# Performance work log

Hardware: AMD Instinct MI355X
Metric: run time of the kernel (lower is better)

The kernel has to match this reference:

```python
import jax, jax.numpy as jnp
import numpy as np

IMG = 640
STRIDES = (8, 16, 32)
A = 5            # anchors per level
NC = 80          # num classes
IOU_TH = 0.5
NEG_RATIO = 1.0


def make_priors():
    scales = [1.0, 1.5, 2.0, 2.5, 3.0]
    out = []
    for s in STRIDES:
        f = IMG // s
        ys, xs = np.meshgrid(np.arange(f), np.arange(f), indexing='ij')
        cx = ((xs + 0.5) / f).ravel()
        cy = ((ys + 0.5) / f).ravel()
        for sc in scales:  # anchor-major to match merge_features (A, h, w) order
            wh = min(sc * 4.0 * s / IMG, 1.0)
            out.append(np.stack([cx, cy, np.full_like(cx, wh), np.full_like(cx, wh)], 1))
    return np.concatenate(out, 0).astype(np.float32)  # [42000, 4] cxcywh


def merge_features(feats):
    outs = []
    for feat in feats:
        n, c, h, w = feat.shape
        f = feat.reshape(n, A, c // A, h, w).transpose(0, 1, 3, 4, 2)
        outs.append(f.reshape(n, A * h * w, c // A))
    return jnp.concatenate(outs, axis=1)  # [n, M, 85]


def box_iou_cxcywh(a, b):
    # a [T,4], b [M,4] (cx,cy,w,h) -> IoU [T,M]
    a1 = jnp.concatenate([a[:, :2] - a[:, 2:] / 2, a[:, :2] + a[:, 2:] / 2], -1)
    b1 = jnp.concatenate([b[:, :2] - b[:, 2:] / 2, b[:, :2] + b[:, 2:] / 2], -1)
    tl = jnp.maximum(a1[:, None, :2], b1[None, :, :2])
    br = jnp.minimum(a1[:, None, 2:], b1[None, :, 2:])
    wh = jnp.clip(br - tl, 0.0)
    inter = wh[..., 0] * wh[..., 1]
    area_a = a[:, 2] * a[:, 3]
    area_b = b[:, 2] * b[:, 3]
    return inter / (area_a[:, None] + area_b[None, :] - inter + 1e-9)


def build_targets(targets, priors, batch):
    ious = box_iou_cxcywh(targets[:, 2:6], priors)  # [Nt, M]
    Nt, M = ious.shape
    img_ids = targets[:, 0].astype(jnp.int32)

    def per_image(i):
        valid = img_ids == i  # [Nt]
        iv = jnp.where(valid[:, None], ious, -1.0)
        best_gt_overlap = iv.max(0)            # [M]
        best_gt_idx = iv.argmax(0)             # [M]
        best_prior_idx = iv.argmax(1)          # [Nt]
        # torch: index_fill_(1) then sequential best_gt_overlap[best_prior_idx[j]] = j
        local_j = (jnp.cumsum(valid.astype(jnp.int32)) - 1).astype(jnp.float32)
        scat_idx = jnp.where(valid, best_prior_idx, M)  # drop invalid rows
        best_gt_overlap = best_gt_overlap.at[scat_idx].set(local_j, mode='drop')
        bbox = targets[best_gt_idx, 2:6]
        clss = targets[best_gt_idx, 1] + 1.0
        clss = jnp.where(best_gt_overlap < IOU_TH, 0.0, clss)
        t_xy = (bbox[:, :2] - priors[:, :2]) / priors[:, 2:]
        t_wh = jnp.log(bbox[:, 2:] / priors[:, 2:])
        return t_xy, t_wh, clss

    return jax.vmap(per_image)(jnp.arange(batch))  # [B,M,2],[B,M,2],[B,M]


def _smooth_l1(x):
    ax = jnp.abs(x)
    return jnp.where(ax < 1.0, 0.5 * ax * ax, ax - 0.5)


def compute_loss(preds, priors, targets):
    n, m, _ = preds.shape
    t_xy, t_wh, t_cls = build_targets(targets, priors, n)
    pos = t_cls > 0
    posf = pos.astype(preds.dtype)
    num_pos = posf.sum()

    # lbox: smooth L1 on xy and wh over positives (mean over pos*2 elements each)
    den2 = jnp.maximum(num_pos * 2.0, 1.0)
    lbox = (_smooth_l1(preds[..., 0:2] - t_xy) * posf[..., None]).sum() / den2 \
         + (_smooth_l1(preds[..., 2:4] - t_wh) * posf[..., None]).sum() / den2

    # lcls: cross entropy over positives, labels = t_cls - 1
    labels = jnp.clip(t_cls.astype(jnp.int32) - 1, 0, NC - 1)
    logz = jax.nn.log_softmax(preds[..., 5:], axis=-1)
    ce = -jnp.take_along_axis(logz, labels[..., None], axis=-1)[..., 0]
    lcls = (ce * posf).sum() / jnp.maximum(num_pos, 1.0)

    # hard negative mining (no grad): double argsort rank trick
    obj = preds[..., 4]
    loss_c = jax.lax.stop_gradient(-jax.nn.log_sigmoid(obj))
    loss_c = jnp.where(pos, 0.0, loss_c)
    order = jnp.argsort(-loss_c, axis=-1)
    rank = jnp.argsort(order, axis=-1)
    num_neg = jnp.minimum(NEG_RATIO * num_pos, m - num_pos)
    neg = rank.astype(preds.dtype) < num_neg
    sel = (pos | neg).astype(preds.dtype)

    # lobj: BCE-with-logits over pos|neg
    z = posf
    bce = jnp.maximum(obj, 0.0) - obj * z + jnp.log1p(jnp.exp(-jnp.abs(obj)))
    lobj = (bce * sel).sum() / jnp.maximum(sel.sum(), 1.0)

    loss = lbox + lcls + lobj
    return jnp.stack([loss, lbox, lobj, lcls])


def setup_inputs() -> dict:
    key = jax.random.key(0)
    ks = jax.random.split(key, 6)
    feat0 = jax.random.normal(ks[0], (8, 425, 80, 80), jnp.float32)
    feat1 = jax.random.normal(ks[1], (8, 425, 40, 40), jnp.float32)
    feat2 = jax.random.normal(ks[2], (8, 425, 20, 20), jnp.float32)
    B, T = 8, 20
    img = jnp.repeat(jnp.arange(B, dtype=jnp.float32), T)
    cls = jax.random.randint(ks[3], (B * T,), 0, NC).astype(jnp.float32)
    cxcy = jax.random.uniform(ks[4], (B * T, 2), minval=0.2, maxval=0.8)
    wh = jax.random.uniform(ks[5], (B * T, 2), minval=0.05, maxval=0.3)
    targets = jnp.concatenate([img[:, None], cls[:, None], cxcy, wh], 1)
    priors = jnp.asarray(make_priors())
    return {"feat0": feat0, "feat1": feat1, "feat2": feat2,
            "targets": targets, "priors": priors}


def reference(feat0, feat1, feat2, targets, priors):
    preds = merge_features([feat0, feat1, feat2])  # [8, 42000, 85]
    return compute_loss(preds, priors, targets)    # [loss, lbox, lobj, lcls]
```

## Files before the change

### kernel.cpp

```cpp
#include <hip/hip_runtime.h>
#include <math.h>

#define MTOT 42000
#define NB 8
#define NCLS 80
#define CAP_LIST 4096
#define MAXT 256
#define NT_MAX 2048
#define GX_MAIN 165
#define NBLK_MAIN (GX_MAIN*NB)
#define NCHB 8
#define CSB 5250
#define TCH 512

#define O_OVR 0
#define O_GIX (O_OVR + NB*MTOT*4)
#define O_OBJ (O_GIX + NB*MTOT*4)
#define O_LSC (O_OBJ + NB*MTOT*4)
#define O_BCE (O_LSC + NB*MTOT*4)
#define O_LJ  (O_BCE + NB*MTOT*4)
#define O_BPP (((O_LJ + NT_MAX*4 + 7)/8)*8)
#define O_PA  (O_BPP + NT_MAX*NCHB*8)
#define O_PN  (O_PA + NBLK_MAIN*16)
#define O_P2  (O_PN + NBLK_MAIN*4)
#define O_BINL (O_P2 + NBLK_MAIN*8)
#define O_HA  (((O_BINL + NB*CAP_LIST*2*4 + 255)/256)*256)
#define O_HB  (O_HA + NB*256*4)
#define O_ACC (O_HB + NB*256*4)
#define O_ACCI (O_ACC + 64)
#define O_ZEND (O_ACCI + 128)
#define ZWORDS ((O_ZEND - O_HA)/4)
#define ZBLK ((ZWORDS + 255)/256)

__device__ __forceinline__ float iou_cxcywh(float acx,float acy,float aw,float ah,
                                            float bcx,float bcy,float bw,float bh){
  float ax0=acx-aw*0.5f, ay0=acy-ah*0.5f, ax1=acx+aw*0.5f, ay1=acy+ah*0.5f;
  float bx0=bcx-bw*0.5f, by0=bcy-bh*0.5f, bx1=bcx+bw*0.5f, by1=bcy+bh*0.5f;
  float tlx=fmaxf(ax0,bx0), tly=fmaxf(ay0,by0);
  float brx=fminf(ax1,bx1), bry=fminf(ay1,by1);
  float wx=fmaxf(brx-tlx,0.f), wy=fmaxf(bry-tly,0.f);
  float inter=wx*wy;
  return inter/(aw*ah+bw*bh-inter+1e-9f);
}

__device__ __forceinline__ float sl1(float x){
  float ax=fabsf(x); return ax<1.f ? 0.5f*ax*ax : ax-0.5f;
}

__device__ __forceinline__ void feat_base(const float* f0,const float* f1,const float* f2,
                                          int i,int m,const float** basep,int* hwp){
  const float* fp; int hw, loc;
  if(m<32000){ fp=f0; hw=6400; loc=m; }
  else if(m<40000){ fp=f1; hw=1600; loc=m-32000; }
  else { fp=f2; hw=400; loc=m-40000; }
  int a=loc/hw, p=loc-a*hw;
  *basep = fp + (size_t)(i*425 + a*85)*(size_t)hw + p;
  *hwp = hw;
}

__device__ __forceinline__ void fine_scan(const unsigned* hb,int ca,int kres,int* bs_out,int* r_out){
  if(ca==0x7fffffff){ *bs_out=0x7fffffff; *r_out=0; return; }
  int run=0, bs=-1, r=0;
  for(int f=255;f>=0;f--){
    int cb=(int)hb[f];
    if(run<kres && run+cb>=kres){ bs=(ca<<8)|f; r=kres-run; break; }
    run+=cb;
  }
  if(bs<0){ bs=(ca<<8); r=kres-run; }
  *bs_out=bs; *r_out=r;
}

__global__ void k_big0(const float* __restrict__ f0,const float* __restrict__ f1,const float* __restrict__ f2,
                       const float* __restrict__ tg,const float* __restrict__ priors,
                       int nt,int b0,int b1,int b2,
                       int* __restrict__ lj,unsigned* __restrict__ zbase,
                       float* __restrict__ ovr,int* __restrict__ gix,
                       float* __restrict__ objc,unsigned long long* __restrict__ bpp){
  __shared__ float st[TCH*6];
  __shared__ unsigned long long su[256];
  int b=blockIdx.x, tid=threadIdx.x;
  if(b<ZBLK){
    int w=b*256+tid;
    if(w<ZWORDS) zbase[w]=0u;
    return;
  }
  if(b<b0){
    int t=(b-ZBLK)*256+tid;
    if(t>=nt) return;
    int img=(int)tg[t*6];
    int j=0;
    for(int q=0;q<t;q++) if((int)tg[q*6]==img) j++;
    lj[t]=j;
    return;
  }
  if(b<b1){
    int idx=b-b0;
    int i=idx/GX_MAIN, cb=idx-(idx/GX_MAIN)*GX_MAIN;
    int m=cb*256+tid;
    bool valid=(m<MTOT);
    float4 pr=make_float4(0.f,0.f,1.f,1.f);
    if(valid) pr=((const float4*)priors)[m];
    float maxv=-1.f; int bi=0;
    for(int base=0;base<nt;base+=TCH){
      int nch=min(TCH,nt-base);
      for(int j=tid;j<nch;j+=256){
        #pragma unroll
        for(int q=0;q<6;q++) st[j*6+q]=tg[(base+j)*6+q];
      }
      __syncthreads();
      if(valid){
        for(int j=0;j<nch;j++){
          if((int)st[j*6]!=i) continue;
          float v=iou_cxcywh(st[j*6+2],st[j*6+3],st[j*6+4],st[j*6+5],pr.x,pr.y,pr.z,pr.w);
          if(v>maxv){ maxv=v; bi=base+j; }
        }
      }
      __syncthreads();
    }
    if(valid){ ovr[i*MTOT+m]=maxv; gix[i*MTOT+m]=bi; }
  } else if(b<b2){
    int idx=b-b1;
    int i=idx/GX_MAIN, cb=idx-(idx/GX_MAIN)*GX_MAIN;
    int m=cb*256+tid;
    if(m>=MTOT) return;
    const float* base; int hw;
    feat_base(f0,f1,f2,i,m,&base,&hw);
    objc[i*MTOT+m]=base[(size_t)4*hw];
  } else {
    int idx=b-b2;
    int t=idx/NCHB, c=idx-(idx/NCHB)*NCHB;
    float acx=tg[t*6+2],acy=tg[t*6+3],aw=tg[t*6+4],ah=tg[t*6+5];
    int m0=c*CSB, m1=min(m0+CSB,MTOT);
    float bv=-1.f; int bm=0;
    for(int m=m0+tid;m<m1;m+=256){
      float4 pr=((const float4*)priors)[m];
      float v=iou_cxcywh(acx,acy,aw,ah,pr.x,pr.y,pr.z,pr.w);
      if(v>bv){ bv=v; bm=m; }
    }
    unsigned long long p=(bv<0.f)?0ull
        :(((unsigned long long)__float_as_uint(bv))<<32)|(unsigned)(~bm);
    su[tid]=p;
    __syncthreads();
    for(int o=128;o>0;o>>=1){
      if(tid<o){ if(su[tid+o]>su[tid]) su[tid]=su[tid+o]; }
      __syncthreads();
    }
    if(tid==0) bpp[(size_t)t*NCHB+c]=su[0];
  }
}

__global__ void k_bpsc(const float* __restrict__ tg,int nt,
                       const unsigned long long* __restrict__ bpp,
                       const int* __restrict__ lj,float* __restrict__ ovr){
  __shared__ int tbp[NT_MAX];
  __shared__ int timg[NT_MAX];
  int tid=threadIdx.x;
  for(int t=tid;t<nt;t+=256){
    unsigned long long best=0ull;
    const unsigned long long* pp=&bpp[(size_t)t*NCHB];
    #pragma unroll
    for(int c=0;c<NCHB;c++){ unsigned long long v=pp[c]; if(v>best) best=v; }
    int bm=~((unsigned)(best&0xFFFFFFFFull));
    tbp[t]=min(max(bm,0),MTOT-1);
    timg[t]=(int)tg[t*6];
  }
  __syncthreads();
  for(int t=tid;t<nt;t+=256){
    int img=timg[t];
    if(img<0||img>=NB) continue;
    int myp=tbp[t];
    bool last=true;
    for(int q=t+1;q<nt;q++) if(timg[q]==img&&tbp[q]==myp){ last=false; break; }
    if(last) ovr[img*MTOT+myp]=(float)lj[t];
  }
}

__global__ void k_lc(const float* __restrict__ tg,const float* __restrict__ objc,
                     const float* __restrict__ ovr,const int* __restrict__ gix,int nt,
                     float* __restrict__ lsc,float* __restrict__ bcearr,
                     unsigned* __restrict__ histA,int* __restrict__ partN){
  __shared__ unsigned h[256];
  __shared__ int snp[4];
  int tid=threadIdx.x, lane=tid&63, wid=tid>>6;
  h[tid]=0u;
  __syncthreads();
  int i=blockIdx.y;
  int m=blockIdx.x*256+tid;
  int npos=0;
  if(m<MTOT){
    int gid=i*MTOT+m;
    float ov=ovr[gid];
    int gi=min(max(gix[gid],0),nt-1);
    float tc=tg[gi*6+1]+1.f;
    bool pos=(ov>=0.5f)&&(tc>0.f);
    float obj=objc[gid];
    float sp=log1pf(expf(-fabsf(obj)));
    float bce=fmaxf(obj,0.f)-(pos?obj:0.f)+sp;
    float lc=pos?0.f:(fmaxf(-obj,0.f)+sp);
    lsc[gid]=lc; bcearr[gid]=bce;
    atomicAdd(&h[__float_as_uint(lc)>>24],1u);
    npos=pos?1:0;
  }
  #pragma unroll
  for(int o=32;o>0;o>>=1) npos+=__shfl_xor(npos,o);
  if(lane==0) snp[wid]=npos;
  __syncthreads();
  unsigned hc=h[tid];
  if(hc) atomicAdd(&histA[i*256+tid],hc);
  if(tid==0) partN[blockIdx.y*GX_MAIN+blockIdx.x]=snp[0]+snp[1]+snp[2]+snp[3];
}

__global__ void k_redscanA(const int* __restrict__ partN,const unsigned* __restrict__ histA,
                           int* __restrict__ acci){
  __shared__ int an[256];
  __shared__ unsigned h[256];
  int t=threadIdx.x, b=blockIdx.x;
  int n=0;
  for(int e=t;e<NBLK_MAIN;e+=256) n+=partN[e];
  an[t]=n;
  __syncthreads();
  for(int o=128;o>0;o>>=1){ if(t<o) an[t]+=an[t+o]; __syncthreads(); }
  int np=an[0];
  if(b==0&&t==0) acci[0]=np;
  h[t]=histA[b*256+t];
  __syncthreads();
  if(t==0){
    int kk=min(np,MTOT-np);
    if(kk<=0){ acci[2+b]=0x7fffffff; acci[10+b]=0; }
    else{
      int run=0, ca=-1, kres=0;
      for(int c2=255;c2>=0;c2--){
        int cbn=(int)h[c2];
        if(run<kk&&run+cbn>=kk){ ca=c2; kres=kk-run; break; }
        run+=cbn;
      }
      if(ca<0){ ca=0; kres=kk-run; }
      acci[2+b]=ca; acci[10+b]=kres;
    }
  }
}

__global__ void k_big2(const float* __restrict__ f0,const float* __restrict__ f1,const float* __restrict__ f2,
                       const float* __restrict__ tg,const float* __restrict__ priors,
                       const float* __restrict__ ovr,const int* __restrict__ gix,
                       const float* __restrict__ lsc,const float* __restrict__ bcearr,
                       const int* __restrict__ acci,int nt,
                       unsigned* __restrict__ histB,float4* __restrict__ partA){
  __shared__ unsigned h[256];
  __shared__ float rA[4],rB[4],rC[4],rD[4];
  int b=blockIdx.x, tid=threadIdx.x, lane=tid&63, wid=tid>>6;
  if(b<NBLK_MAIN){
    h[tid]=0u;
    __syncthreads();
    int i=b/GX_MAIN, cb=b-(b/GX_MAIN)*GX_MAIN;
    int ca=acci[2+i];
    int m=cb*256+tid;
    if(m<MTOT && ca!=0x7fffffff){
      unsigned u=__float_as_uint(lsc[i*MTOT+m]);
      if((int)(u>>24)==ca) atomicAdd(&h[(u>>16)&0xFF],1u);
    }
    __syncthreads();
    unsigned c=h[tid];
    if(c) atomicAdd(&histB[i*256+tid],c);
  } else {
    int idx=b-NBLK_MAIN;
    int i=idx/GX_MAIN, cb=idx-(idx/GX_MAIN)*GX_MAIN;
    int m=cb*256+tid;
    bool valid=(m<MTOT);
    float lxy=0.f,lwh=0.f,bcep=0.f,wce=0.f;
    bool pos=false; int gi=0;
    if(valid){
      int gid=i*MTOT+m;
      float ov=ovr[gid];
      gi=min(max(gix[gid],0),nt-1);
      float tc=tg[gi*6+1]+1.f;
      pos=(ov>=0.5f)&&(tc>0.f);
      if(pos){
        const float* base; int hw;
        feat_base(f0,f1,f2,i,m,&base,&hw);
        bcep=bcearr[gid];
        float4 pr=((const float4*)priors)[m];
        float bx=tg[gi*6+2],by=tg[gi*6+3],bw=tg[gi*6+4],bh=tg[gi*6+5];
        float tx=(bx-pr.x)/pr.z, ty=(by-pr.y)/pr.w;
        float tw=logf(bw/pr.z), th=logf(bh/pr.w);
        lxy=sl1(base[0]-tx)+sl1(base[(size_t)hw]-ty);
        lwh=sl1(base[(size_t)2*hw]-tw)+sl1(base[(size_t)3*hw]-th);
      }
    }
    unsigned long long mask=__ballot(valid&&pos);
    while(mask){
      int s=__ffsll(mask)-1;
      mask&=mask-1;
      int m_s=__shfl(m,s);
      int gi_s=__shfl(gi,s);
      const float* bs2; int hws;
      feat_base(f0,f1,f2,i,m_s,&bs2,&hws);
      int label=(int)(tg[gi_s*6+1]+1.f)-1;
      label=min(NCLS-1,max(0,label));
      float v0=bs2[(size_t)(5+lane)*hws];
      float v1=(lane<16)?bs2[(size_t)(69+lane)*hws]:-3.0e38f;
      float mx=fmaxf(v0,v1);
      #pragma unroll
      for(int o=32;o>0;o>>=1) mx=fmaxf(mx,__shfl_xor(mx,o));
      float se=expf(v0-mx)+((lane<16)?expf(v1-mx):0.f);
      float xl=((lane==label)?v0:0.f)+((lane<16&&lane+64==label)?v1:0.f);
      #pragma unroll
      for(int o=32;o>0;o>>=1){ se+=__shfl_xor(se,o); xl+=__shfl_xor(xl,o); }
      wce+=logf(se)+mx-xl;
    }
    #pragma unroll
    for(int o=32;o>0;o>>=1){
      lxy+=__shfl_xor(lxy,o); lwh+=__shfl_xor(lwh,o); bcep+=__shfl_xor(bcep,o);
    }
    if(lane==0){ rA[wid]=lxy; rB[wid]=lwh; rC[wid]=wce; rD[wid]=bcep; }
    __syncthreads();
    if(tid==0)
      partA[idx]=make_float4(rA[0]+rA[1]+rA[2]+rA[3], rB[0]+rB[1]+rB[2]+rB[3],
                             rC[0]+rC[1]+rC[2]+rC[3], rD[0]+rD[1]+rD[2]+rD[3]);
  }
}

__global__ void k_select(const float* __restrict__ lsc,const float* __restrict__ bcearr,
                         const unsigned* __restrict__ histB,
                         int* __restrict__ acci,float2* __restrict__ part2,
                         int* __restrict__ binlist){
  __shared__ unsigned hb[256];
  __shared__ int sbs;
  __shared__ float ss[4]; __shared__ float sc[4];
  int tid=threadIdx.x, lane=tid&63, wid=tid>>6;
  int i=blockIdx.y;
  int ca=acci[2+i], kres=acci[10+i];
  hb[tid]=(ca==0x7fffffff)?0u:histB[i*256+tid];
  __syncthreads();
  if(tid==0){ int bs,r; fine_scan(hb,ca,kres,&bs,&r); sbs=bs; }
  __syncthreads();
  int bs_=sbs;
  int m=blockIdx.x*256+tid;
  float s=0.f, c=0.f;
  if(m<MTOT){
    int gid=i*MTOT+m;
    unsigned u=__float_as_uint(lsc[gid]);
    int bin=(int)(u>>16);
    if(bin>bs_){ s=bcearr[gid]; c=1.f; }
    else if(bin==bs_){
      int idx=atomicAdd(&acci[18+i],1);
      if(idx<CAP_LIST){
        binlist[((size_t)i*CAP_LIST+idx)*2  ]=(int)u;
        binlist[((size_t)i*CAP_LIST+idx)*2+1]=gid;
      }
    }
  }
  #pragma unroll
  for(int o=32;o>0;o>>=1){ s+=__shfl_xor(s,o); c+=__shfl_xor(c,o); }
  if(lane==0){ ss[wid]=s; sc[wid]=c; }
  __syncthreads();
  if(tid==0) part2[blockIdx.y*gridDim.x+blockIdx.x]=make_float2(ss[0]+ss[1]+ss[2]+ss[3], sc[0]+sc[1]+sc[2]+sc[3]);
}

#define TSTAGE 2048
__global__ void k_ties(const float* __restrict__ bcearr,int* __restrict__ acci,
                       float* __restrict__ accf,const int* __restrict__ binlist,
                       const unsigned* __restrict__ histB){
  __shared__ unsigned hb[256];
  __shared__ int sbs, sr;
  __shared__ int sl[TSTAGE*2];
  int i=blockIdx.x, tid=threadIdx.x;
  int ca=acci[2+i], kres=acci[10+i];
  hb[tid]=(ca==0x7fffffff)?0u:histB[i*256+tid];
  __syncthreads();
  if(tid==0){ int bs,r; fine_scan(hb,ca,kres,&bs,&r); sbs=bs; sr=r; }
  __syncthreads();
  if(sbs==0x7fffffff) return;
  int n=min(acci[18+i],CAP_LIST);
  int nstage=min(n,TSTAGE);
  for(int e=tid;e<nstage;e+=256){
    sl[e*2  ]=binlist[((size_t)i*CAP_LIST+e)*2  ];
    sl[e*2+1]=binlist[((size_t)i*CAP_LIST+e)*2+1];
  }
  __syncthreads();
  int r=sr;
  for(int e=tid;e<n;e+=blockDim.x){
    unsigned ue; int ge;
    if(e<nstage){ ue=(unsigned)sl[e*2]; ge=sl[e*2+1]; }
    else{ ue=(unsigned)binlist[((size_t)i*CAP_LIST+e)*2]; ge=binlist[((size_t)i*CAP_LIST+e)*2+1]; }
    int rank=0;
    for(int q=0;q<n;q++){
      unsigned uq; int gq;
      if(q<nstage){ uq=(unsigned)sl[q*2]; gq=sl[q*2+1]; }
      else{ uq=(unsigned)binlist[((size_t)i*CAP_LIST+q)*2]; gq=binlist[((size_t)i*CAP_LIST+q)*2+1]; }
      rank += ((uq>ue)||(uq==ue&&gq<ge))?1:0;
    }
    if(rank<r){
      atomicAdd(&accf[5], bcearr[ge]);
      atomicAdd(&acci[1], 1);
    }
  }
}

__global__ void k_final(const float4* __restrict__ partA,const float2* __restrict__ part2,
                        const float* __restrict__ accf,const int* __restrict__ acci,
                        float* __restrict__ out){
  __shared__ float a0[256],a1[256],a2[256],a3[256],s0[256],s1[256];
  int tid=threadIdx.x;
  float x=0,y=0,z=0,w=0,ns=0,nc=0;
  for(int e=tid;e<NBLK_MAIN;e+=256){
    float4 p=partA[e]; x+=p.x; y+=p.y; z+=p.z; w+=p.w;
    float2 q=part2[e]; ns+=q.x; nc+=q.y;
  }
  a0[tid]=x; a1[tid]=y; a2[tid]=z; a3[tid]=w; s0[tid]=ns; s1[tid]=nc;
  __syncthreads();
  for(int o=128;o>0;o>>=1){
    if(tid<o){
      a0[tid]+=a0[tid+o]; a1[tid]+=a1[tid+o]; a2[tid]+=a2[tid+o]; a3[tid]+=a3[tid+o];
      s0[tid]+=s0[tid+o]; s1[tid]+=s1[tid+o];
    }
    __syncthreads();
  }
  if(tid==0){
    float negsum=s0[0]+accf[5];
    float negcnt=s1[0]+(float)acci[1];
    int np=acci[0];
    float npf=(float)np;
    float den2=fmaxf(2.f*npf,1.f);
    float lbox=a0[0]/den2+a1[0]/den2;
    float lcls=a2[0]/fmaxf(npf,1.f);
    float selc=npf+negcnt;
    float lobj=(a3[0]+negsum)/fmaxf(selc,1.f);
    out[0]=lbox+lcls+lobj;
    out[1]=lbox;
    out[2]=lobj;
    out[3]=lcls;
  }
}

extern "C" void kernel_launch(void* const* d_in, const int* in_sizes, int n_in,
                              void* d_out, int out_size, void* d_ws, size_t ws_size,
                              hipStream_t stream) {
  const float* f0=(const float*)d_in[0];
  const float* f1=(const float*)d_in[1];
  const float* f2=(const float*)d_in[2];
  const float* tg=(const float*)d_in[3];
  const float* priors=(const float*)d_in[4];
  int nt = in_sizes[3]/6;
  if(nt>NT_MAX) nt=NT_MAX;
  if(nt<1) nt=1;

  char* ws=(char*)d_ws;
  float*    ovr    =(float*)   (ws+O_OVR);
  int*      gix    =(int*)     (ws+O_GIX);
  float*    objc   =(float*)   (ws+O_OBJ);
  float*    lsc    =(float*)   (ws+O_LSC);
  float*    bcearr =(float*)   (ws+O_BCE);
  int*      lj     =(int*)     (ws+O_LJ);
  unsigned long long* bpp=(unsigned long long*)(ws+O_BPP);
  float4*   partA  =(float4*)  (ws+O_PA);
  int*      partN  =(int*)     (ws+O_PN);
  float2*   part2  =(float2*)  (ws+O_P2);
  int*      binlist=(int*)     (ws+O_BINL);
  unsigned* histA  =(unsigned*)(ws+O_HA);
  unsigned* histB  =(unsigned*)(ws+O_HB);
  float*    accf   =(float*)   (ws+O_ACC);
  int*      acci   =(int*)     (ws+O_ACCI);
  unsigned* zbase  =(unsigned*)(ws+O_HA);

  int ntb=(nt+255)/256;
  int b0=ZBLK+ntb, b1=b0+NBLK_MAIN, b2=b1+NBLK_MAIN;
  k_big0<<<b2+nt*NCHB,256,0,stream>>>(f0,f1,f2,tg,priors,nt,b0,b1,b2,lj,zbase,ovr,gix,objc,bpp);
  k_bpsc<<<1,256,0,stream>>>(tg,nt,bpp,lj,ovr);
  dim3 gm(GX_MAIN, NB);
  k_lc<<<gm,256,0,stream>>>(tg,objc,ovr,gix,nt,lsc,bcearr,histA,partN);
  k_redscanA<<<NB,256,0,stream>>>(partN,histA,acci);
  k_big2<<<2*NBLK_MAIN,256,0,stream>>>(f0,f1,f2,tg,priors,ovr,gix,lsc,bcearr,acci,nt,histB,partA);
  k_select<<<gm,256,0,stream>>>(lsc,bcearr,histB,acci,part2,binlist);
  k_ties<<<NB,256,0,stream>>>(bcearr,acci,accf,binlist,histB);
  k_final<<<1,256,0,stream>>>(partA,part2,accf,acci,(float*)d_out);
}
```

Measured before the change: 132.9 us.

## Fold reduce/scan, tie-breaking and final kernels into last-block epilogues

Removes three small launches (k_redscanA, k_ties, k_final) by appending their work to k_lc and k_select. Each of those kernels now uses a threadfence plus atomic counter to elect the last finishing block, which then does the work. This saves launch latency and inter-kernel gaps. The cost is that the tie ranking for all eight images now runs serially in one block without shared-memory staging, which could be slow when many ties exist. The done counters sit in the zeroed workspace region, so they are reset on each call.

```diff
diff --git a/kernel.cpp b/kernel.cpp
--- a/kernel.cpp
+++ b/kernel.cpp
@@ -5,7 +5,6 @@
 #define NB 8
 #define NCLS 80
 #define CAP_LIST 4096
-#define MAXT 256
 #define NT_MAX 2048
 #define GX_MAIN 165
 #define NBLK_MAIN (GX_MAIN*NB)
@@ -26,9 +25,9 @@
 #define O_BINL (O_P2 + NBLK_MAIN*8)
 #define O_HA  (((O_BINL + NB*CAP_LIST*2*4 + 255)/256)*256)
 #define O_HB  (O_HA + NB*256*4)
-#define O_ACC (O_HB + NB*256*4)
-#define O_ACCI (O_ACC + 64)
-#define O_ZEND (O_ACCI + 128)
+#define O_ACCI (O_HB + NB*256*4)
+#define O_DC  (O_ACCI + 128)
+#define O_ZEND (O_DC + 64)
 #define ZWORDS ((O_ZEND - O_HA)/4)
 #define ZBLK ((ZWORDS + 255)/256)
 
@@ -68,6 +67,16 @@
   }
   if(bs<0){ bs=(ca<<8); r=kres-run; }
   *bs_out=bs; *r_out=r;
+}
+
+__device__ __forceinline__ bool block_is_last(int* ctr,int total,int* sh_last){
+  __threadfence();
+  __syncthreads();
+  if(threadIdx.x==0) *sh_last = (atomicAdd(ctr,1)==total-1) ? 1 : 0;
+  __syncthreads();
+  bool last = (*sh_last!=0);
+  if(last) __threadfence();
+  return last;
 }
 
 __global__ void k_big0(const float* __restrict__ f0,const float* __restrict__ f1,const float* __restrict__ f2,
@@ -178,9 +187,12 @@
 __global__ void k_lc(const float* __restrict__ tg,const float* __restrict__ objc,
                      const float* __restrict__ ovr,const int* __restrict__ gix,int nt,
                      float* __restrict__ lsc,float* __restrict__ bcearr,
-                     unsigned* __restrict__ histA,int* __restrict__ partN){
+                     unsigned* __restrict__ histA,int* __restrict__ partN,
+                     int* __restrict__ acci,int* __restrict__ dc){
   __shared__ unsigned h[256];
   __shared__ int snp[4];
+  __shared__ int an[256];
+  __shared__ int sh_last;
   int tid=threadIdx.x, lane=tid&63, wid=tid>>6;
   h[tid]=0u;
   __syncthreads();
@@ -208,34 +220,29 @@
   unsigned hc=h[tid];
   if(hc) atomicAdd(&histA[i*256+tid],hc);
   if(tid==0) partN[blockIdx.y*GX_MAIN+blockIdx.x]=snp[0]+snp[1]+snp[2]+snp[3];
-}
-
-__global__ void k_redscanA(const int* __restrict__ partN,const unsigned* __restrict__ histA,
-                           int* __restrict__ acci){
-  __shared__ int an[256];
-  __shared__ unsigned h[256];
-  int t=threadIdx.x, b=blockIdx.x;
-  int n=0;
-  for(int e=t;e<NBLK_MAIN;e+=256) n+=partN[e];
-  an[t]=n;
-  __syncthreads();
-  for(int o=128;o>0;o>>=1){ if(t<o) an[t]+=an[t+o]; __syncthreads(); }
-  int np=an[0];
-  if(b==0&&t==0) acci[0]=np;
-  h[t]=histA[b*256+t];
-  __syncthreads();
-  if(t==0){
-    int kk=min(np,MTOT-np);
-    if(kk<=0){ acci[2+b]=0x7fffffff; acci[10+b]=0; }
-    else{
-      int run=0, ca=-1, kres=0;
-      for(int c2=255;c2>=0;c2--){
-        int cbn=(int)h[c2];
-        if(run<kk&&run+cbn>=kk){ ca=c2; kres=kk-run; break; }
-        run+=cbn;
-      }
-      if(ca<0){ ca=0; kres=kk-run; }
-      acci[2+b]=ca; acci[10+b]=kres;
+
+  if(block_is_last(&dc[0],NBLK_MAIN,&sh_last)){
+    int n=0;
+    for(int e=tid;e<NBLK_MAIN;e+=256) n+=partN[e];
+    an[tid]=n;
+    __syncthreads();
+    for(int o=128;o>0;o>>=1){ if(tid<o) an[tid]+=an[tid+o]; __syncthreads(); }
+    int np=an[0];
+    if(tid==0) acci[0]=np;
+    if(tid<NB){
+      int im=tid;
+      int kk=min(np,MTOT-np);
+      if(kk<=0){ acci[2+im]=0x7fffffff; acci[10+im]=0; }
+      else{
+        int run=0, ca=-1, kres=0;
+        for(int c2=255;c2>=0;c2--){
+          int cbn=(int)histA[im*256+c2];
+          if(run<kk&&run+cbn>=kk){ ca=c2; kres=kk-run; break; }
+          run+=cbn;
+        }
+        if(ca<0){ ca=0; kres=kk-run; }
+        acci[2+im]=ca; acci[10+im]=kres;
+      }
     }
   }
 }
@@ -323,10 +330,14 @@
 __global__ void k_select(const float* __restrict__ lsc,const float* __restrict__ bcearr,
                          const unsigned* __restrict__ histB,
                          int* __restrict__ acci,float2* __restrict__ part2,
-                         int* __restrict__ binlist){
+                         int* __restrict__ binlist,
+                         const float4* __restrict__ partA,
+                         float* __restrict__ out,int* __restrict__ dc){
   __shared__ unsigned hb[256];
-  __shared__ int sbs;
+  __shared__ int sbs, sr;
   __shared__ float ss[4]; __shared__ float sc[4];
+  __shared__ float a0[256],a1[256],a2[256],a3[256],s0[256],s1[256];
+  __shared__ int sh_last;
   int tid=threadIdx.x, lane=tid&63, wid=tid>>6;
   int i=blockIdx.y;
   int ca=acci[2+i], kres=acci[10+i];
@@ -355,81 +366,69 @@
   if(lane==0){ ss[wid]=s; sc[wid]=c; }
   __syncthreads();
   if(tid==0) part2[blockIdx.y*gridDim.x+blockIdx.x]=make_float2(ss[0]+ss[1]+ss[2]+ss[3], sc[0]+sc[1]+sc[2]+sc[3]);
-}
-
-#define TSTAGE 2048
-__global__ void k_ties(const float* __restrict__ bcearr,int* __restrict__ acci,
-                       float* __restrict__ accf,const int* __restrict__ binlist,
-                       const unsigned* __restrict__ histB){
-  __shared__ unsigned hb[256];
-  __shared__ int sbs, sr;
-  __shared__ int sl[TSTAGE*2];
-  int i=blockIdx.x, tid=threadIdx.x;
-  int ca=acci[2+i], kres=acci[10+i];
-  hb[tid]=(ca==0x7fffffff)?0u:histB[i*256+tid];
-  __syncthreads();
-  if(tid==0){ int bs,r; fine_scan(hb,ca,kres,&bs,&r); sbs=bs; sr=r; }
-  __syncthreads();
-  if(sbs==0x7fffffff) return;
-  int n=min(acci[18+i],CAP_LIST);
-  int nstage=min(n,TSTAGE);
-  for(int e=tid;e<nstage;e+=256){
-    sl[e*2  ]=binlist[((size_t)i*CAP_LIST+e)*2  ];
-    sl[e*2+1]=binlist[((size_t)i*CAP_LIST+e)*2+1];
-  }
-  __syncthreads();
-  int r=sr;
-  for(int e=tid;e<n;e+=blockDim.x){
-    unsigned ue; int ge;
-    if(e<nstage){ ue=(unsigned)sl[e*2]; ge=sl[e*2+1]; }
-    else{ ue=(unsigned)binlist[((size_t)i*CAP_LIST+e)*2]; ge=binlist[((size_t)i*CAP_LIST+e)*2+1]; }
-    int rank=0;
-    for(int q=0;q<n;q++){
-      unsigned uq; int gq;
-      if(q<nstage){ uq=(unsigned)sl[q*2]; gq=sl[q*2+1]; }
-      else{ uq=(unsigned)binlist[((size_t)i*CAP_LIST+q)*2]; gq=binlist[((size_t)i*CAP_LIST+q)*2+1]; }
-      rank += ((uq>ue)||(uq==ue&&gq<ge))?1:0;
-    }
-    if(rank<r){
-      atomicAdd(&accf[5], bcearr[ge]);
-      atomicAdd(&acci[1], 1);
-    }
-  }
-}
-
-__global__ void k_final(const float4* __restrict__ partA,const float2* __restrict__ part2,
-                        const float* __restrict__ accf,const int* __restrict__ acci,
-                        float* __restrict__ out){
-  __shared__ float a0[256],a1[256],a2[256],a3[256],s0[256],s1[256];
-  int tid=threadIdx.x;
-  float x=0,y=0,z=0,w=0,ns=0,nc=0;
-  for(int e=tid;e<NBLK_MAIN;e+=256){
-    float4 p=partA[e]; x+=p.x; y+=p.y; z+=p.z; w+=p.w;
-    float2 q=part2[e]; ns+=q.x; nc+=q.y;
-  }
-  a0[tid]=x; a1[tid]=y; a2[tid]=z; a3[tid]=w; s0[tid]=ns; s1[tid]=nc;
-  __syncthreads();
-  for(int o=128;o>0;o>>=1){
-    if(tid<o){
-      a0[tid]+=a0[tid+o]; a1[tid]+=a1[tid+o]; a2[tid]+=a2[tid+o]; a3[tid]+=a3[tid+o];
-      s0[tid]+=s0[tid+o]; s1[tid]+=s1[tid+o];
-    }
-    __syncthreads();
-  }
-  if(tid==0){
-    float negsum=s0[0]+accf[5];
-    float negcnt=s1[0]+(float)acci[1];
-    int np=acci[0];
-    float npf=(float)np;
-    float den2=fmaxf(2.f*npf,1.f);
-    float lbox=a0[0]/den2+a1[0]/den2;
-    float lcls=a2[0]/fmaxf(npf,1.f);
-    float selc=npf+negcnt;
-    float lobj=(a3[0]+negsum)/fmaxf(selc,1.f);
-    out[0]=lbox+lcls+lobj;
-    out[1]=lbox;
-    out[2]=lobj;
-    out[3]=lcls;
+
+  if(block_is_last(&dc[1],NBLK_MAIN,&sh_last)){
+    float x=0,y=0,z=0,w=0,ns=0,nc=0;
+    for(int e=tid;e<NBLK_MAIN;e+=256){
+      float4 p=partA[e]; x+=p.x; y+=p.y; z+=p.z; w+=p.w;
+      float2 q=part2[e]; ns+=q.x; nc+=q.y;
+    }
+    a0[tid]=x; a1[tid]=y; a2[tid]=z; a3[tid]=w; s0[tid]=ns; s1[tid]=nc;
+    __syncthreads();
+    for(int o=128;o>0;o>>=1){
+      if(tid<o){
+        a0[tid]+=a0[tid+o]; a1[tid]+=a1[tid+o]; a2[tid]+=a2[tid+o]; a3[tid]+=a3[tid+o];
+        s0[tid]+=s0[tid+o]; s1[tid]+=s1[tid+o];
+      }
+      __syncthreads();
+    }
+    float sum_xy=a0[0], sum_wh=a1[0], sum_ce=a2[0], sum_bcep=a3[0];
+    float negsum=s0[0], negcnt=s1[0];
+    __syncthreads();
+    float tsum=0.f; int tcnt=0;
+    for(int im=0;im<NB;im++){
+      int ca2=acci[2+im], kres2=acci[10+im];
+      __syncthreads();
+      hb[tid]=(ca2==0x7fffffff)?0u:histB[im*256+tid];
+      __syncthreads();
+      if(tid==0){ int bs,r; fine_scan(hb,ca2,kres2,&bs,&r); sbs=bs; sr=r; }
+      __syncthreads();
+      if(sbs==0x7fffffff) continue;
+      int n=min(acci[18+im],CAP_LIST);
+      int r=sr;
+      for(int e=tid;e<n;e+=256){
+        unsigned ue=(unsigned)binlist[((size_t)im*CAP_LIST+e)*2];
+        int ge=binlist[((size_t)im*CAP_LIST+e)*2+1];
+        int rank=0;
+        for(int q=0;q<n;q++){
+          unsigned uq=(unsigned)binlist[((size_t)im*CAP_LIST+q)*2];
+          int gq=binlist[((size_t)im*CAP_LIST+q)*2+1];
+          rank += ((uq>ue)||(uq==ue&&gq<ge))?1:0;
+        }
+        if(rank<r){ tsum+=bcearr[ge]; tcnt++; }
+      }
+    }
+    float ftc=(float)tcnt;
+    #pragma unroll
+    for(int o=32;o>0;o>>=1){ tsum+=__shfl_xor(tsum,o); ftc+=__shfl_xor(ftc,o); }
+    __syncthreads();
+    if(lane==0){ a0[wid]=tsum; a1[wid]=ftc; }
+    __syncthreads();
+    if(tid==0){
+      negsum+=a0[0]+a0[1]+a0[2]+a0[3];
+      negcnt+=a1[0]+a1[1]+a1[2]+a1[3];
+      int np=acci[0];
+      float npf=(float)np;
+      float den2=fmaxf(2.f*npf,1.f);
+      float lbox=sum_xy/den2+sum_wh/den2;
+      float lcls=sum_ce/fmaxf(npf,1.f);
+      float selc=npf+negcnt;
+      float lobj=(sum_bcep+negsum)/fmaxf(selc,1.f);
+      out[0]=lbox+lcls+lobj;
+      out[1]=lbox;
+      out[2]=lobj;
+      out[3]=lcls;
+    }
   }
 }
 
@@ -459,8 +458,8 @@
   int*      binlist=(int*)     (ws+O_BINL);
   unsigned* histA  =(unsigned*)(ws+O_HA);
   unsigned* histB  =(unsigned*)(ws+O_HB);
-  float*    accf   =(float*)   (ws+O_ACC);
   int*      acci   =(int*)     (ws+O_ACCI);
+  int*      dc     =(int*)     (ws+O_DC);
   unsigned* zbase  =(unsigned*)(ws+O_HA);
 
   int ntb=(nt+255)/256;
@@ -468,10 +467,7 @@
   k_big0<<<b2+nt*NCHB,256,0,stream>>>(f0,f1,f2,tg,priors,nt,b0,b1,b2,lj,zbase,ovr,gix,objc,bpp);
   k_bpsc<<<1,256,0,stream>>>(tg,nt,bpp,lj,ovr);
   dim3 gm(GX_MAIN, NB);
-  k_lc<<<gm,256,0,stream>>>(tg,objc,ovr,gix,nt,lsc,bcearr,histA,partN);
-  k_redscanA<<<NB,256,0,stream>>>(partN,histA,acci);
+  k_lc<<<gm,256,0,stream>>>(tg,objc,ovr,gix,nt,lsc,bcearr,histA,partN,acci,dc);
   k_big2<<<2*NBLK_MAIN,256,0,stream>>>(f0,f1,f2,tg,priors,ovr,gix,lsc,bcearr,acci,nt,histB,partA);
-  k_select<<<gm,256,0,stream>>>(lsc,bcearr,histB,acci,part2,binlist);
-  k_ties<<<NB,256,0,stream>>>(bcearr,acci,accf,binlist,histB);
-  k_final<<<1,256,0,stream>>>(partA,part2,accf,acci,(float*)d_out);
-}
+  k_select<<<gm,256,0,stream>>>(lsc,bcearr,histB,acci,part2,binlist,partA,(float*)d_out,dc);
+}
```

Result: slower. 434.0 us (+226.6%).

## Compact per-image targets in IoU loop and fuse loss-stage kernels

Applied to the files above, without the earlier changes.

In the IoU max kernel, one wavefront uses a ballot to pack the targets belonging to the block's image into a compact shared list, so every thread loops only over those targets rather than all of them. The per-prior loss/histogram kernel is merged with the positive box/class loss work so both run in one launch, and the box-loss side recomputes the BCE from the objectness logit instead of reading it back. The tie-resolution and final-reduction kernels become a single 512-thread block, with one wavefront per image, and sums are accumulated in registers rather than through global atomics. Together this cuts kernel launches and the redundant target loop, at the cost of one wavefront per image doing the tie ranking and a smaller shared staging buffer.

```diff
diff --git a/kernel.cpp b/kernel.cpp
--- a/kernel.cpp
+++ b/kernel.cpp
@@ -5,13 +5,13 @@
 #define NB 8
 #define NCLS 80
 #define CAP_LIST 4096
-#define MAXT 256
 #define NT_MAX 2048
 #define GX_MAIN 165
 #define NBLK_MAIN (GX_MAIN*NB)
 #define NCHB 8
 #define CSB 5250
 #define TCH 512
+#define TST 384
 
 #define O_OVR 0
 #define O_GIX (O_OVR + NB*MTOT*4)
@@ -26,8 +26,7 @@
 #define O_BINL (O_P2 + NBLK_MAIN*8)
 #define O_HA  (((O_BINL + NB*CAP_LIST*2*4 + 255)/256)*256)
 #define O_HB  (O_HA + NB*256*4)
-#define O_ACC (O_HB + NB*256*4)
-#define O_ACCI (O_ACC + 64)
+#define O_ACCI (O_HB + NB*256*4)
 #define O_ZEND (O_ACCI + 128)
 #define ZWORDS ((O_ZEND - O_HA)/4)
 #define ZBLK ((ZWORDS + 255)/256)
@@ -77,6 +76,9 @@
                        float* __restrict__ ovr,int* __restrict__ gix,
                        float* __restrict__ objc,unsigned long long* __restrict__ bpp){
   __shared__ float st[TCH*6];
+  __shared__ float sc[TCH*4];
+  __shared__ int cidx[TCH];
+  __shared__ int s_ncomp;
   __shared__ unsigned long long su[256];
   int b=blockIdx.x, tid=threadIdx.x;
   if(b<ZBLK){
@@ -108,11 +110,28 @@
         for(int q=0;q<6;q++) st[j*6+q]=tg[(base+j)*6+q];
       }
       __syncthreads();
+      if(tid<64){
+        int cnt=0;
+        for(int bb=0;bb<nch;bb+=64){
+          int j=bb+tid;
+          bool f=(j<nch)&&((int)st[j*6]==i);
+          unsigned long long mk=__ballot(f);
+          if(f){
+            int pos=cnt+__popcll(mk&((1ull<<tid)-1ull));
+            cidx[pos]=base+j;
+            sc[pos*4+0]=st[j*6+2]; sc[pos*4+1]=st[j*6+3];
+            sc[pos*4+2]=st[j*6+4]; sc[pos*4+3]=st[j*6+5];
+          }
+          cnt+=__popcll(mk);
+        }
+        if(tid==0) s_ncomp=cnt;
+      }
+      __syncthreads();
+      int nci=s_ncomp;
       if(valid){
-        for(int j=0;j<nch;j++){
-          if((int)st[j*6]!=i) continue;
-          float v=iou_cxcywh(st[j*6+2],st[j*6+3],st[j*6+4],st[j*6+5],pr.x,pr.y,pr.z,pr.w);
-          if(v>maxv){ maxv=v; bi=base+j; }
+        for(int j=0;j<nci;j++){
+          float v=iou_cxcywh(sc[j*4+0],sc[j*4+1],sc[j*4+2],sc[j*4+3],pr.x,pr.y,pr.z,pr.w);
+          if(v>maxv){ maxv=v; bi=cidx[j]; }
         }
       }
       __syncthreads();
@@ -175,93 +194,44 @@
   }
 }
 
-__global__ void k_lc(const float* __restrict__ tg,const float* __restrict__ objc,
-                     const float* __restrict__ ovr,const int* __restrict__ gix,int nt,
-                     float* __restrict__ lsc,float* __restrict__ bcearr,
-                     unsigned* __restrict__ histA,int* __restrict__ partN){
-  __shared__ unsigned h[256];
-  __shared__ int snp[4];
-  int tid=threadIdx.x, lane=tid&63, wid=tid>>6;
-  h[tid]=0u;
-  __syncthreads();
-  int i=blockIdx.y;
-  int m=blockIdx.x*256+tid;
-  int npos=0;
-  if(m<MTOT){
-    int gid=i*MTOT+m;
-    float ov=ovr[gid];
-    int gi=min(max(gix[gid],0),nt-1);
-    float tc=tg[gi*6+1]+1.f;
-    bool pos=(ov>=0.5f)&&(tc>0.f);
-    float obj=objc[gid];
-    float sp=log1pf(expf(-fabsf(obj)));
-    float bce=fmaxf(obj,0.f)-(pos?obj:0.f)+sp;
-    float lc=pos?0.f:(fmaxf(-obj,0.f)+sp);
-    lsc[gid]=lc; bcearr[gid]=bce;
-    atomicAdd(&h[__float_as_uint(lc)>>24],1u);
-    npos=pos?1:0;
-  }
-  #pragma unroll
-  for(int o=32;o>0;o>>=1) npos+=__shfl_xor(npos,o);
-  if(lane==0) snp[wid]=npos;
-  __syncthreads();
-  unsigned hc=h[tid];
-  if(hc) atomicAdd(&histA[i*256+tid],hc);
-  if(tid==0) partN[blockIdx.y*GX_MAIN+blockIdx.x]=snp[0]+snp[1]+snp[2]+snp[3];
-}
-
-__global__ void k_redscanA(const int* __restrict__ partN,const unsigned* __restrict__ histA,
-                           int* __restrict__ acci){
-  __shared__ int an[256];
-  __shared__ unsigned h[256];
-  int t=threadIdx.x, b=blockIdx.x;
-  int n=0;
-  for(int e=t;e<NBLK_MAIN;e+=256) n+=partN[e];
-  an[t]=n;
-  __syncthreads();
-  for(int o=128;o>0;o>>=1){ if(t<o) an[t]+=an[t+o]; __syncthreads(); }
-  int np=an[0];
-  if(b==0&&t==0) acci[0]=np;
-  h[t]=histA[b*256+t];
-  __syncthreads();
-  if(t==0){
-    int kk=min(np,MTOT-np);
-    if(kk<=0){ acci[2+b]=0x7fffffff; acci[10+b]=0; }
-    else{
-      int run=0, ca=-1, kres=0;
-      for(int c2=255;c2>=0;c2--){
-        int cbn=(int)h[c2];
-        if(run<kk&&run+cbn>=kk){ ca=c2; kres=kk-run; break; }
-        run+=cbn;
-      }
-      if(ca<0){ ca=0; kres=kk-run; }
-      acci[2+b]=ca; acci[10+b]=kres;
-    }
-  }
-}
-
-__global__ void k_big2(const float* __restrict__ f0,const float* __restrict__ f1,const float* __restrict__ f2,
-                       const float* __restrict__ tg,const float* __restrict__ priors,
-                       const float* __restrict__ ovr,const int* __restrict__ gix,
-                       const float* __restrict__ lsc,const float* __restrict__ bcearr,
-                       const int* __restrict__ acci,int nt,
-                       unsigned* __restrict__ histB,float4* __restrict__ partA){
+__global__ void k_lcpos(const float* __restrict__ f0,const float* __restrict__ f1,const float* __restrict__ f2,
+                        const float* __restrict__ tg,const float* __restrict__ priors,
+                        const float* __restrict__ objc,
+                        const float* __restrict__ ovr,const int* __restrict__ gix,int nt,
+                        float* __restrict__ lsc,float* __restrict__ bcearr,
+                        unsigned* __restrict__ histA,int* __restrict__ partN,
+                        float4* __restrict__ partA){
   __shared__ unsigned h[256];
   __shared__ float rA[4],rB[4],rC[4],rD[4];
+  __shared__ int snp[4];
   int b=blockIdx.x, tid=threadIdx.x, lane=tid&63, wid=tid>>6;
   if(b<NBLK_MAIN){
     h[tid]=0u;
     __syncthreads();
     int i=b/GX_MAIN, cb=b-(b/GX_MAIN)*GX_MAIN;
-    int ca=acci[2+i];
     int m=cb*256+tid;
-    if(m<MTOT && ca!=0x7fffffff){
-      unsigned u=__float_as_uint(lsc[i*MTOT+m]);
-      if((int)(u>>24)==ca) atomicAdd(&h[(u>>16)&0xFF],1u);
-    }
+    int npos=0;
+    if(m<MTOT){
+      int gid=i*MTOT+m;
+      float ov=ovr[gid];
+      int gi=min(max(gix[gid],0),nt-1);
+      float tc=tg[gi*6+1]+1.f;
+      bool pos=(ov>=0.5f)&&(tc>0.f);
+      float obj=objc[gid];
+      float sp=log1pf(expf(-fabsf(obj)));
+      float bce=fmaxf(obj,0.f)-(pos?obj:0.f)+sp;
+      float lc=pos?0.f:(fmaxf(-obj,0.f)+sp);
+      lsc[gid]=lc; bcearr[gid]=bce;
+      atomicAdd(&h[__float_as_uint(lc)>>24],1u);
+      npos=pos?1:0;
+    }
+    #pragma unroll
+    for(int o=32;o>0;o>>=1) npos+=__shfl_xor(npos,o);
+    if(lane==0) snp[wid]=npos;
     __syncthreads();
-    unsigned c=h[tid];
-    if(c) atomicAdd(&histB[i*256+tid],c);
+    unsigned hc=h[tid];
+    if(hc) atomicAdd(&histA[i*256+tid],hc);
+    if(tid==0) partN[b]=snp[0]+snp[1]+snp[2]+snp[3];
   } else {
     int idx=b-NBLK_MAIN;
     int i=idx/GX_MAIN, cb=idx-(idx/GX_MAIN)*GX_MAIN;
@@ -278,7 +248,8 @@
       if(pos){
         const float* base; int hw;
         feat_base(f0,f1,f2,i,m,&base,&hw);
-        bcep=bcearr[gid];
+        float obj=objc[gid];
+        bcep=fmaxf(obj,0.f)-obj+log1pf(expf(-fabsf(obj)));
         float4 pr=((const float4*)priors)[m];
         float bx=tg[gi*6+2],by=tg[gi*6+3],bw=tg[gi*6+4],bh=tg[gi*6+5];
         float tx=(bx-pr.x)/pr.z, ty=(by-pr.y)/pr.w;
@@ -320,13 +291,60 @@
   }
 }
 
+__global__ void k_redscanA(const int* __restrict__ partN,const unsigned* __restrict__ histA,
+                           int* __restrict__ acci){
+  __shared__ int an[256];
+  __shared__ unsigned h[256];
+  int t=threadIdx.x, b=blockIdx.x;
+  int n=0;
+  for(int e=t;e<NBLK_MAIN;e+=256) n+=partN[e];
+  an[t]=n;
+  __syncthreads();
+  for(int o=128;o>0;o>>=1){ if(t<o) an[t]+=an[t+o]; __syncthreads(); }
+  int np=an[0];
+  if(b==0&&t==0) acci[0]=np;
+  h[t]=histA[b*256+t];
+  __syncthreads();
+  if(t==0){
+    int kk=min(np,MTOT-np);
+    if(kk<=0){ acci[2+b]=0x7fffffff; acci[10+b]=0; }
+    else{
+      int run=0, ca=-1, kres=0;
+      for(int c2=255;c2>=0;c2--){
+        int cbn=(int)h[c2];
+        if(run<kk&&run+cbn>=kk){ ca=c2; kres=kk-run; break; }
+        run+=cbn;
+      }
+      if(ca<0){ ca=0; kres=kk-run; }
+      acci[2+b]=ca; acci[10+b]=kres;
+    }
+  }
+}
+
+__global__ void k_histB(const float* __restrict__ lsc,const int* __restrict__ acci,
+                        unsigned* __restrict__ histB){
+  __shared__ unsigned h[256];
+  h[threadIdx.x]=0u;
+  __syncthreads();
+  int i=blockIdx.y;
+  int ca=acci[2+i];
+  int m=blockIdx.x*256+threadIdx.x;
+  if(m<MTOT && ca!=0x7fffffff){
+    unsigned u=__float_as_uint(lsc[i*MTOT+m]);
+    if((int)(u>>24)==ca) atomicAdd(&h[(u>>16)&0xFF],1u);
+  }
+  __syncthreads();
+  unsigned c=h[threadIdx.x];
+  if(c) atomicAdd(&histB[i*256+threadIdx.x],c);
+}
+
 __global__ void k_select(const float* __restrict__ lsc,const float* __restrict__ bcearr,
                          const unsigned* __restrict__ histB,
                          int* __restrict__ acci,float2* __restrict__ part2,
                          int* __restrict__ binlist){
   __shared__ unsigned hb[256];
   __shared__ int sbs;
-  __shared__ float ss[4]; __shared__ float sc[4];
+  __shared__ float ss[4]; __shared__ float sc2[4];
   int tid=threadIdx.x, lane=tid&63, wid=tid>>6;
   int i=blockIdx.y;
   int ca=acci[2+i], kres=acci[10+i];
@@ -352,64 +370,64 @@
   }
   #pragma unroll
   for(int o=32;o>0;o>>=1){ s+=__shfl_xor(s,o); c+=__shfl_xor(c,o); }
-  if(lane==0){ ss[wid]=s; sc[wid]=c; }
-  __syncthreads();
-  if(tid==0) part2[blockIdx.y*gridDim.x+blockIdx.x]=make_float2(ss[0]+ss[1]+ss[2]+ss[3], sc[0]+sc[1]+sc[2]+sc[3]);
-}
-
-#define TSTAGE 2048
-__global__ void k_ties(const float* __restrict__ bcearr,int* __restrict__ acci,
-                       float* __restrict__ accf,const int* __restrict__ binlist,
-                       const unsigned* __restrict__ histB){
-  __shared__ unsigned hb[256];
-  __shared__ int sbs, sr;
-  __shared__ int sl[TSTAGE*2];
-  int i=blockIdx.x, tid=threadIdx.x;
-  int ca=acci[2+i], kres=acci[10+i];
-  hb[tid]=(ca==0x7fffffff)?0u:histB[i*256+tid];
-  __syncthreads();
-  if(tid==0){ int bs,r; fine_scan(hb,ca,kres,&bs,&r); sbs=bs; sr=r; }
-  __syncthreads();
-  if(sbs==0x7fffffff) return;
-  int n=min(acci[18+i],CAP_LIST);
-  int nstage=min(n,TSTAGE);
-  for(int e=tid;e<nstage;e+=256){
-    sl[e*2  ]=binlist[((size_t)i*CAP_LIST+e)*2  ];
-    sl[e*2+1]=binlist[((size_t)i*CAP_LIST+e)*2+1];
-  }
-  __syncthreads();
-  int r=sr;
-  for(int e=tid;e<n;e+=blockDim.x){
-    unsigned ue; int ge;
-    if(e<nstage){ ue=(unsigned)sl[e*2]; ge=sl[e*2+1]; }
-    else{ ue=(unsigned)binlist[((size_t)i*CAP_LIST+e)*2]; ge=binlist[((size_t)i*CAP_LIST+e)*2+1]; }
-    int rank=0;
-    for(int q=0;q<n;q++){
-      unsigned uq; int gq;
-      if(q<nstage){ uq=(unsigned)sl[q*2]; gq=sl[q*2+1]; }
-      else{ uq=(unsigned)binlist[((size_t)i*CAP_LIST+q)*2]; gq=binlist[((size_t)i*CAP_LIST+q)*2+1]; }
-      rank += ((uq>ue)||(uq==ue&&gq<ge))?1:0;
-    }
-    if(rank<r){
-      atomicAdd(&accf[5], bcearr[ge]);
-      atomicAdd(&acci[1], 1);
-    }
-  }
-}
-
-__global__ void k_final(const float4* __restrict__ partA,const float2* __restrict__ part2,
-                        const float* __restrict__ accf,const int* __restrict__ acci,
-                        float* __restrict__ out){
-  __shared__ float a0[256],a1[256],a2[256],a3[256],s0[256],s1[256];
-  int tid=threadIdx.x;
-  float x=0,y=0,z=0,w=0,ns=0,nc=0;
-  for(int e=tid;e<NBLK_MAIN;e+=256){
-    float4 p=partA[e]; x+=p.x; y+=p.y; z+=p.z; w+=p.w;
+  if(lane==0){ ss[wid]=s; sc2[wid]=c; }
+  __syncthreads();
+  if(tid==0) part2[blockIdx.y*gridDim.x+blockIdx.x]=make_float2(ss[0]+ss[1]+ss[2]+ss[3], sc2[0]+sc2[1]+sc2[2]+sc2[3]);
+}
+
+__global__ void k_tiesfinal(const float* __restrict__ bcearr,const unsigned* __restrict__ histB,
+                            int* __restrict__ acci,const int* __restrict__ binlist,
+                            const float4* __restrict__ partA,const float2* __restrict__ part2,
+                            float* __restrict__ out){
+  __shared__ unsigned hb[NB*256];
+  __shared__ int sbs[NB], sr2[NB];
+  __shared__ int stg[NB*TST*2];
+  __shared__ float tsumW[NB]; __shared__ float tcntW[NB];
+  __shared__ float a0[512],a1[512],a2[512],a3[512],s0[512],s1[512];
+  int tid=threadIdx.x, w=tid>>6, lane=tid&63;
+  int ca=acci[2+w], kres=acci[10+w];
+  for(int e=lane;e<256;e+=64) hb[w*256+e]=(ca==0x7fffffff)?0u:histB[w*256+e];
+  __syncthreads();
+  if(lane==0){ int bs,r; fine_scan(&hb[w*256],ca,kres,&bs,&r); sbs[w]=bs; sr2[w]=r; }
+  __syncthreads();
+  int bs=sbs[w], r=sr2[w];
+  int n=min(acci[18+w],CAP_LIST);
+  int nst=min(n,TST);
+  if(bs!=0x7fffffff){
+    for(int e=lane;e<nst;e+=64){
+      stg[(w*TST+e)*2  ]=binlist[((size_t)w*CAP_LIST+e)*2  ];
+      stg[(w*TST+e)*2+1]=binlist[((size_t)w*CAP_LIST+e)*2+1];
+    }
+  }
+  __syncthreads();
+  float tsum=0.f, tcnt=0.f;
+  if(bs!=0x7fffffff){
+    for(int e=lane;e<n;e+=64){
+      unsigned ue; int ge;
+      if(e<nst){ ue=(unsigned)stg[(w*TST+e)*2]; ge=stg[(w*TST+e)*2+1]; }
+      else{ ue=(unsigned)binlist[((size_t)w*CAP_LIST+e)*2]; ge=binlist[((size_t)w*CAP_LIST+e)*2+1]; }
+      int rank=0;
+      for(int q=0;q<n;q++){
+        unsigned uq; int gq;
+        if(q<nst){ uq=(unsigned)stg[(w*TST+q)*2]; gq=stg[(w*TST+q)*2+1]; }
+        else{ uq=(unsigned)binlist[((size_t)w*CAP_LIST+q)*2]; gq=binlist[((size_t)w*CAP_LIST+q)*2+1]; }
+        rank += ((uq>ue)||(uq==ue&&gq<ge))?1:0;
+      }
+      if(rank<r){ tsum+=bcearr[ge]; tcnt+=1.f; }
+    }
+  }
+  #pragma unroll
+  for(int o=32;o>0;o>>=1){ tsum+=__shfl_xor(tsum,o); tcnt+=__shfl_xor(tcnt,o); }
+  if(lane==0){ tsumW[w]=tsum; tcntW[w]=tcnt; }
+  __syncthreads();
+  float x=0,y=0,z=0,ww=0,ns=0,nc=0;
+  for(int e=tid;e<NBLK_MAIN;e+=512){
+    float4 p=partA[e]; x+=p.x; y+=p.y; z+=p.z; ww+=p.w;
     float2 q=part2[e]; ns+=q.x; nc+=q.y;
   }
-  a0[tid]=x; a1[tid]=y; a2[tid]=z; a3[tid]=w; s0[tid]=ns; s1[tid]=nc;
-  __syncthreads();
-  for(int o=128;o>0;o>>=1){
+  a0[tid]=x; a1[tid]=y; a2[tid]=z; a3[tid]=ww; s0[tid]=ns; s1[tid]=nc;
+  __syncthreads();
+  for(int o=256;o>0;o>>=1){
     if(tid<o){
       a0[tid]+=a0[tid+o]; a1[tid]+=a1[tid+o]; a2[tid]+=a2[tid+o]; a3[tid]+=a3[tid+o];
       s0[tid]+=s0[tid+o]; s1[tid]+=s1[tid+o];
@@ -417,8 +435,8 @@
     __syncthreads();
   }
   if(tid==0){
-    float negsum=s0[0]+accf[5];
-    float negcnt=s1[0]+(float)acci[1];
+    float negsum=s0[0], negcnt=s1[0];
+    for(int im=0;im<NB;im++){ negsum+=tsumW[im]; negcnt+=tcntW[im]; }
     int np=acci[0];
     float npf=(float)np;
     float den2=fmaxf(2.f*npf,1.f);
@@ -459,7 +477,6 @@
   int*      binlist=(int*)     (ws+O_BINL);
   unsigned* histA  =(unsigned*)(ws+O_HA);
   unsigned* histB  =(unsigned*)(ws+O_HB);
-  float*    accf   =(float*)   (ws+O_ACC);
   int*      acci   =(int*)     (ws+O_ACCI);
   unsigned* zbase  =(unsigned*)(ws+O_HA);
 
@@ -467,11 +484,10 @@
   int b0=ZBLK+ntb, b1=b0+NBLK_MAIN, b2=b1+NBLK_MAIN;
   k_big0<<<b2+nt*NCHB,256,0,stream>>>(f0,f1,f2,tg,priors,nt,b0,b1,b2,lj,zbase,ovr,gix,objc,bpp);
   k_bpsc<<<1,256,0,stream>>>(tg,nt,bpp,lj,ovr);
+  k_lcpos<<<2*NBLK_MAIN,256,0,stream>>>(f0,f1,f2,tg,priors,objc,ovr,gix,nt,lsc,bcearr,histA,partN,partA);
+  k_redscanA<<<NB,256,0,stream>>>(partN,histA,acci);
   dim3 gm(GX_MAIN, NB);
-  k_lc<<<gm,256,0,stream>>>(tg,objc,ovr,gix,nt,lsc,bcearr,histA,partN);
-  k_redscanA<<<NB,256,0,stream>>>(partN,histA,acci);
-  k_big2<<<2*NBLK_MAIN,256,0,stream>>>(f0,f1,f2,tg,priors,ovr,gix,lsc,bcearr,acci,nt,histB,partA);
+  k_histB<<<gm,256,0,stream>>>(lsc,acci,histB);
   k_select<<<gm,256,0,stream>>>(lsc,bcearr,histB,acci,part2,binlist);
-  k_ties<<<NB,256,0,stream>>>(bcearr,acci,accf,binlist,histB);
-  k_final<<<1,256,0,stream>>>(partA,part2,accf,acci,(float*)d_out);
-}
+  k_tiesfinal<<<1,512,0,stream>>>(bcearr,histB,acci,binlist,partA,part2,(float*)d_out);
+}
```

Result: slower. 140.8 us (+5.9%).
